# Kernel optimization log

Hardware: AMD Instinct MI355X
Metric: run time of the kernel (lower is better)

## Reference

```python
import jax, jax.numpy as jnp
import numpy as np

B, S, D, H = 4, 2048, 1024, 16
HD = D // H
EPS = 1e-5

def layernorm(x, g, b):
    mu = jnp.mean(x, axis=-1, keepdims=True)
    var = jnp.mean((x - mu) ** 2, axis=-1, keepdims=True)
    return (x - mu) * jax.lax.rsqrt(var + EPS) * g + b

def setup_inputs() -> dict:
    key = jax.random.key(0)
    ks = jax.random.split(key, 12)
    s = 0.02
    return {
        "x": jax.random.normal(ks[0], (B, S, D), dtype=jnp.float32),
        "g1": jnp.ones((D,), jnp.float32), "beta1": jnp.zeros((D,), jnp.float32),
        "Wq": jax.random.normal(ks[1], (H, HD, HD), jnp.float32) * s,
        "bq": jnp.zeros((H, HD), jnp.float32),
        "Wk": jax.random.normal(ks[2], (H, HD, HD), jnp.float32) * s,
        "bk": jnp.zeros((H, HD), jnp.float32),
        "Wv": jax.random.normal(ks[3], (H, HD, HD), jnp.float32) * s,
        "bv": jnp.zeros((H, HD), jnp.float32),
        "Wp": jax.random.normal(ks[4], (D, D), jnp.float32) * s,
        "bp": jnp.zeros((D,), jnp.float32),
        "g2": jnp.ones((D,), jnp.float32), "beta2": jnp.zeros((D,), jnp.float32),
        "W1": jax.random.normal(ks[5], (4 * D, D), jnp.float32) * s,
        "b1": jnp.zeros((4 * D,), jnp.float32),
        "W2": jax.random.normal(ks[6], (D, 4 * D), jnp.float32) * s,
        "b2": jnp.zeros((D,), jnp.float32),
    }

def reference(x, g1, beta1, Wq, bq, Wk, bk, Wv, bv, Wp, bp, g2, beta2, W1, b1, W2, b2):
    # pre-norm
    h = layernorm(x, g1, beta1)              # [B,S,D]
    hh = h.reshape(B, S, H, HD)              # per-head slices of d_model
    # per-head linear: y = x @ W.T + b (torch Linear convention)
    q = jnp.einsum('bshd,hed->bshe', hh, Wq) + bq
    k = jnp.einsum('bshd,hed->bshe', hh, Wk) + bk
    v = jnp.einsum('bshd,hed->bshe', hh, Wv) + bv
    scores = jnp.einsum('bshe,bthe->bhst', q, k) / jnp.sqrt(jnp.float32(HD))
    causal = jnp.tril(jnp.ones((S, S), bool))
    scores = jnp.where(causal, scores, -jnp.inf)
    w = jax.nn.softmax(scores, axis=-1)      # [B,H,S,S]
    attn = jnp.einsum('bhst,bthd->bshd', w, v).reshape(B, S, D)
    out = attn @ Wp.T + bp
    x = x + out
    h2 = layernorm(x, g2, beta2)
    ff = jax.nn.gelu(h2 @ W1.T + b1, approximate=False) @ W2.T + b2
    return x + ff
```

## Files before the change

### kernel.cpp

```cpp
#include <hip/hip_runtime.h>

#define TOK 8192
#define DMODEL 1024
#define NHEAD 16
#define SEQ 2048
#define HDIM 64
#define NQB 16

typedef __attribute__((ext_vector_type(8))) short short8;
typedef __attribute__((ext_vector_type(4))) float f32x4;

__device__ __forceinline__ ushort f2bf(float f){
  unsigned int u = __float_as_uint(f);
  u = u + 0x7fffu + ((u >> 16) & 1u);
  return (ushort)(u >> 16);
}

__device__ __forceinline__ void gld16(const void* g, void* l){
  __builtin_amdgcn_global_load_lds((const __attribute__((address_space(1))) unsigned int*)g,
                                   (__attribute__((address_space(3))) unsigned int*)l, 16, 0, 0);
}

__global__ __launch_bounds__(256) void cvt_kernel(const float* __restrict__ src, ushort* __restrict__ dst, int n4){
  int i = blockIdx.x * 256 + threadIdx.x;
  if(i < n4){
    float4 v = ((const float4*)src)[i];
    ushort4 o;
    o.x = f2bf(v.x); o.y = f2bf(v.y); o.z = f2bf(v.z); o.w = f2bf(v.w);
    ((ushort4*)dst)[i] = o;
  }
}

__device__ __forceinline__ float waveRedSum(float v){
  #pragma unroll
  for(int off = 32; off; off >>= 1) v += __shfl_xor(v, off);
  return v;
}

__global__ __launch_bounds__(256) void ln_kernel(const float* __restrict__ x, const float* __restrict__ g,
                                                 const float* __restrict__ bt, ushort* __restrict__ out){
  int row = blockIdx.x, t = threadIdx.x;
  float4 v = ((const float4*)(x + (size_t)row * DMODEL))[t];
  float s  = v.x + v.y + v.z + v.w;
  float sq = v.x*v.x + v.y*v.y + v.z*v.z + v.w*v.w;
  s = waveRedSum(s); sq = waveRedSum(sq);
  __shared__ float ss[4], ssq[4];
  if((t & 63) == 0){ ss[t >> 6] = s; ssq[t >> 6] = sq; }
  __syncthreads();
  float S  = ss[0] + ss[1] + ss[2] + ss[3];
  float SQ = ssq[0] + ssq[1] + ssq[2] + ssq[3];
  float mean = S * (1.f / DMODEL);
  float var  = SQ * (1.f / DMODEL) - mean * mean;
  float rstd = rsqrtf(var + 1e-5f);
  float4 gv = ((const float4*)g)[t];
  float4 bv = ((const float4*)bt)[t];
  ushort4 o;
  o.x = f2bf((v.x - mean) * rstd * gv.x + bv.x);
  o.y = f2bf((v.y - mean) * rstd * gv.y + bv.y);
  o.z = f2bf((v.z - mean) * rstd * gv.z + bv.z);
  o.w = f2bf((v.w - mean) * rstd * gv.w + bv.w);
  ((ushort4*)(out + (size_t)row * DMODEL))[t] = o;
}

__global__ __launch_bounds__(256) void qkv_kernel(const ushort* __restrict__ h, const ushort* __restrict__ wqkv,
                                                  const float* __restrict__ bq, const float* __restrict__ bk,
                                                  const float* __restrict__ bv,
                                                  ushort* __restrict__ q, ushort* __restrict__ k, ushort* __restrict__ vT){
  __shared__ __attribute__((aligned(16))) ushort hs[64 * 72];
  __shared__ __attribute__((aligned(16))) ushort wsh[3][64 * 72];
  int head = blockIdx.y;
  int tb = blockIdx.x * 64;
  int t = threadIdx.x;
  int r = t >> 2, c0 = (t & 3) * 16;
  {
    const uint4* src = (const uint4*)(h + (size_t)(tb + r) * DMODEL + head * 64 + c0);
    uint4 p0 = src[0], p1 = src[1];
    *(uint4*)&hs[r * 72 + c0] = p0;
    *(uint4*)&hs[r * 72 + c0 + 8] = p1;
  }
  #pragma unroll
  for(int o = 0; o < 3; o++){
    const uint4* wsrc = (const uint4*)(wqkv + ((size_t)(o * NHEAD + head) * 64 + r) * 64 + c0);
    uint4 a0 = wsrc[0], a1 = wsrc[1];
    *(uint4*)&wsh[o][r * 72 + c0] = a0;
    *(uint4*)&wsh[o][r * 72 + c0 + 8] = a1;
  }
  __syncthreads();
  int w = t >> 6, l = t & 63, lr = l & 15, lg = l >> 4;
  short8 a0 = *(const short8*)&hs[(w * 16 + lr) * 72 + lg * 8];
  short8 a1 = *(const short8*)&hs[(w * 16 + lr) * 72 + 32 + lg * 8];
  const float* biases[3] = {bq, bk, bv};
  ushort* outs[2] = {q, k};
  #pragma unroll
  for(int o = 0; o < 3; o++){
    #pragma unroll
    for(int nt = 0; nt < 4; nt++){
      f32x4 acc = {0.f, 0.f, 0.f, 0.f};
      short8 b0 = *(const short8*)&wsh[o][(nt * 16 + lr) * 72 + lg * 8];
      short8 b1 = *(const short8*)&wsh[o][(nt * 16 + lr) * 72 + 32 + lg * 8];
      acc = __builtin_amdgcn_mfma_f32_16x16x32_bf16(a0, b0, acc, 0, 0, 0);
      acc = __builtin_amdgcn_mfma_f32_16x16x32_bf16(a1, b1, acc, 0, 0, 0);
      float bias = biases[o][head * 64 + nt * 16 + lr];
      #pragma unroll
      for(int rr = 0; rr < 4; rr++){
        int tok = tb + w * 16 + lg * 4 + rr;
        int b_ = tok >> 11, s_ = tok & (SEQ - 1);
        if(o < 2){
          outs[o][((size_t)(b_ * NHEAD + head) * SEQ + s_) * 64 + nt * 16 + lr] = f2bf(acc[rr] + bias);
        } else {
          vT[((size_t)(b_ * NHEAD + head) * 64 + nt * 16 + lr) * SEQ + s_] = f2bf(acc[rr] + bias);
        }
      }
    }
  }
}

__global__ __launch_bounds__(256) void attn_kernel(const ushort* __restrict__ q, const ushort* __restrict__ k,
                                                   const ushort* __restrict__ vT, ushort* __restrict__ attn){
  __shared__ __attribute__((aligned(16))) ushort kt[2][64 * 64];
  __shared__ __attribute__((aligned(16))) ushort vt[2][64 * 64];
  __shared__ __attribute__((aligned(16))) ushort pt[4 * 32 * 72];
  int lid = blockIdx.y * 16 + blockIdx.x;
  int qb = (NQB - 1) - (lid >> 6);
  int bh = lid & 63;
  int t = threadIdx.x, w = t >> 6, l = t & 63, lr = l & 15, lg = l >> 4;
  size_t base = (size_t)bh * SEQ * 64;
  int b_ = bh >> 4, head = bh & 15;

  int r8 = l >> 3, c8 = l & 7;
  int st_row = 8 * w + r8;
  int st_sc  = ((c8 ^ r8) << 3);
  int st_dst = w * 1024 + l * 16;
  int xm  = (lr & 7) << 3;
  int cb0 = (lg * 8) ^ xm;
  int cb1 = (32 + lg * 8) ^ xm;

  const float C = 0.18033688f;

  int cur = 0;
  int qbase = qb * 128;
  int wrow = qbase + w * 32;

  short8 qf[2][2];
  #pragma unroll
  for(int mt = 0; mt < 2; mt++)
    #pragma unroll
    for(int kc = 0; kc < 2; kc++)
      qf[mt][kc] = *(const short8*)&q[base + (size_t)(wrow + mt * 16 + lr) * 64 + kc * 32 + lg * 8];

  f32x4 acc_o[2][4];
  #pragma unroll
  for(int i = 0; i < 2; i++)
    #pragma unroll
    for(int jj = 0; jj < 4; jj++) acc_o[i][jj] = (f32x4){0.f, 0.f, 0.f, 0.f};
  float m_sw[2] = {-__builtin_inff(), -__builtin_inff()};
  float l_sw[2] = {0.f, 0.f};

  int jmax = (qbase + 128) >> 6;
  {
    const ushort* kp = k + base + (size_t)st_row * 64 + st_sc;
    char* kd = (char*)&kt[cur][0] + st_dst;
    gld16(kp, kd);
    gld16(kp + 32 * 64, kd + 4096);
    const ushort* vp = vT + base + (size_t)st_row * SEQ + st_sc;
    char* vd = (char*)&vt[cur][0] + st_dst;
    gld16(vp, vd);
    gld16(vp + 32 * SEQ, vd + 4096);
  }
  #pragma unroll 1
  for(int j = 0; j < jmax; j++){
    __syncthreads();
    if(j + 1 < jmax){
      int kb2 = (j + 1) * 64;
      const ushort* kp = k + base + (size_t)(kb2 + st_row) * 64 + st_sc;
      char* kd = (char*)&kt[cur ^ 1][0] + st_dst;
      gld16(kp, kd);
      gld16(kp + 32 * 64, kd + 4096);
      const ushort* vp = vT + base + (size_t)st_row * SEQ + kb2 + st_sc;
      char* vd = (char*)&vt[cur ^ 1][0] + st_dst;
      gld16(vp, vd);
      gld16(vp + 32 * SEQ, vd + 4096);
    }
    int kb = j * 64;
    if(kb <= wrow + 31){
      f32x4 sacc[2][4];
      #pragma unroll
      for(int nt = 0; nt < 4; nt++){
        short8 b0 = *(const short8*)&kt[cur][(nt * 16 + lr) * 64 + cb0];
        short8 b1 = *(const short8*)&kt[cur][(nt * 16 + lr) * 64 + cb1];
        #pragma unroll
        for(int mt = 0; mt < 2; mt++){
          f32x4 z = (f32x4){0.f, 0.f, 0.f, 0.f};
          z = __builtin_amdgcn_mfma_f32_16x16x32_bf16(b0, qf[mt][0], z, 0, 0, 0);
          z = __builtin_amdgcn_mfma_f32_16x16x32_bf16(b1, qf[mt][1], z, 0, 0, 0);
          sacc[mt][nt] = z;
        }
      }
      if(kb + 63 > wrow){
        #pragma unroll
        for(int mt = 0; mt < 2; mt++)
          #pragma unroll
          for(int nt = 0; nt < 4; nt++)
            #pragma unroll
            for(int rr = 0; rr < 4; rr++){
              int kcol = kb + nt * 16 + lg * 4 + rr;
              int qrow = wrow + mt * 16 + lr;
              if(kcol > qrow) sacc[mt][nt][rr] = -__builtin_inff();
            }
      }
      #pragma unroll
      for(int mt = 0; mt < 2; mt++){
        float tm = sacc[mt][0][0];
        #pragma unroll
        for(int nt = 0; nt < 4; nt++)
          #pragma unroll
          for(int rr = 0; rr < 4; rr++) tm = fmaxf(tm, sacc[mt][nt][rr]);
        tm = fmaxf(tm, __shfl_xor(tm, 16));
        tm = fmaxf(tm, __shfl_xor(tm, 32));
        float nm = fmaxf(m_sw[mt], tm);
        if(__any((nm - m_sw[mt]) > 44.0f)){
          float sc = exp2f((m_sw[mt] - nm) * C);
          l_sw[mt] *= sc;
          m_sw[mt] = nm;
          #pragma unroll
          for(int rr = 0; rr < 4; rr++){
            float scb = __shfl(sc, lg * 4 + rr, 16);
            #pragma unroll
            for(int nt = 0; nt < 4; nt++) acc_o[mt][nt][rr] *= scb;
          }
        }
        float mC = m_sw[mt] * C;
        float rs = 0.f;
        #pragma unroll
        for(int nt = 0; nt < 4; nt++){
          float p0 = exp2f(fmaf(sacc[mt][nt][0], C, -mC));
          float p1 = exp2f(fmaf(sacc[mt][nt][1], C, -mC));
          float p2 = exp2f(fmaf(sacc[mt][nt][2], C, -mC));
          float p3 = exp2f(fmaf(sacc[mt][nt][3], C, -mC));
          rs += (p0 + p1) + (p2 + p3);
          ushort4 pw;
          pw.x = f2bf(p0); pw.y = f2bf(p1); pw.z = f2bf(p2); pw.w = f2bf(p3);
          *(ushort4*)&pt[w * 2304 + (mt * 16 + lr) * 72 + nt * 16 + lg * 4] = pw;
        }
        rs += __shfl_xor(rs, 16);
        rs += __shfl_xor(rs, 32);
        l_sw[mt] += rs;
      }
      #pragma unroll
      for(int kc = 0; kc < 2; kc++){
        short8 pf[2];
        #pragma unroll
        for(int mt = 0; mt < 2; mt++)
          pf[mt] = *(const short8*)&pt[w * 2304 + (mt * 16 + lr) * 72 + kc * 32 + lg * 8];
        int cb = kc ? cb1 : cb0;
        #pragma unroll
        for(int nt = 0; nt < 4; nt++){
          short8 vb = *(const short8*)&vt[cur][(nt * 16 + lr) * 64 + cb];
          #pragma unroll
          for(int mt = 0; mt < 2; mt++)
            acc_o[mt][nt] = __builtin_amdgcn_mfma_f32_16x16x32_bf16(pf[mt], vb, acc_o[mt][nt], 0, 0, 0);
        }
      }
    }
    cur ^= 1;
  }
  #pragma unroll
  for(int mt = 0; mt < 2; mt++){
    float inv = 1.f / l_sw[mt];
    #pragma unroll
    for(int rr = 0; rr < 4; rr++){
      float invb = __shfl(inv, lg * 4 + rr, 16);
      #pragma unroll
      for(int nt = 0; nt < 4; nt++){
        int s_ = wrow + mt * 16 + lg * 4 + rr;
        attn[((size_t)(b_ * SEQ + s_)) * DMODEL + head * 64 + nt * 16 + lr] = f2bf(acc_o[mt][nt][rr] * invb);
      }
    }
  }
}

__device__ __forceinline__ float gelu_exact(float x){
  return 0.5f * x * (1.f + erff(x * 0.70710678118654752f));
}

template<int EPI>
__global__ __launch_bounds__(512, 2) void gemm3(const ushort* __restrict__ A, const ushort* __restrict__ W,
                                                const float* __restrict__ bias, const float* __restrict__ res,
                                                float* __restrict__ outf, ushort* __restrict__ outb,
                                                int M, int N, int K){
  __shared__ __attribute__((aligned(16))) ushort As[3][256 * 64];
  __shared__ __attribute__((aligned(16))) ushort Bs[3][128 * 64];
  int t = threadIdx.x;
  int nwg = gridDim.x * gridDim.y;
  int id = blockIdx.y * gridDim.x + blockIdx.x;
  int bx = blockIdx.x, by = blockIdx.y;
  if((nwg & 7) == 0){
    int qq = nwg >> 3;
    int sw = (id & 7) * qq + (id >> 3);
    bx = sw % gridDim.x; by = sw / gridDim.x;
  }
  int n0 = bx * 128, m0 = by * 256;
  int w = t >> 6, l = t & 63, lr = l & 15, lg = l >> 4;
  int wm = w >> 1, wn = w & 1;
  int ur = t >> 3, u = t & 7;
  int su = (u ^ (ur & 7)) << 3;

  f32x4 acc[4][4];
  #pragma unroll
  for(int i = 0; i < 4; i++)
    #pragma unroll
    for(int j = 0; j < 4; j++) acc[i][j] = (f32x4){0.f, 0.f, 0.f, 0.f};

  int ktiles = K >> 6;

  auto stage = [&](int tile){
    int b = tile % 3;
    int k0 = tile << 6;
    char* ad = (char*)&As[b][0] + t * 16;
    char* bd = (char*)&Bs[b][0] + t * 16;
    #pragma unroll
    for(int i = 0; i < 4; i++){
      int ra = i * 64 + ur;
      gld16(A + (size_t)(m0 + ra) * K + k0 + su, ad + i * 8192);
    }
    #pragma unroll
    for(int i = 0; i < 2; i++){
      int rb = i * 64 + ur;
      gld16(W + (size_t)(n0 + rb) * K + k0 + su, bd + i * 8192);
    }
  };

  stage(0);
  stage(1);

  int xm = (lr & 7) << 3;
  int arow = wm * 64, brow = wn * 64;

  #pragma unroll 1
  for(int kt = 0; kt < ktiles; kt++){
    int b = kt % 3;
    if(kt + 2 < ktiles) stage(kt + 2);
    int rem = ktiles - 1 - kt;
    __builtin_amdgcn_sched_barrier(0);
    if(rem >= 2)      asm volatile("s_waitcnt vmcnt(12)" ::: "memory");
    else if(rem == 1) asm volatile("s_waitcnt vmcnt(6)" ::: "memory");
    else              asm volatile("s_waitcnt vmcnt(0)" ::: "memory");
    __builtin_amdgcn_sched_barrier(0);
    __builtin_amdgcn_s_barrier();

    short8 af[4][2], bf[4][2];
    #pragma unroll
    for(int mf = 0; mf < 4; mf++)
      #pragma unroll
      for(int kk = 0; kk < 2; kk++)
        af[mf][kk] = *(const short8*)&As[b][(arow + mf * 16 + lr) * 64 + ((kk * 32 + lg * 8) ^ xm)];
    #pragma unroll
    for(int nf = 0; nf < 4; nf++)
      #pragma unroll
      for(int kk = 0; kk < 2; kk++)
        bf[nf][kk] = *(const short8*)&Bs[b][(brow + nf * 16 + lr) * 64 + ((kk * 32 + lg * 8) ^ xm)];

    __builtin_amdgcn_s_setprio(1);
    #pragma unroll
    for(int mf = 0; mf < 4; mf++)
      #pragma unroll
      for(int nf = 0; nf < 4; nf++){
        acc[mf][nf] = __builtin_amdgcn_mfma_f32_16x16x32_bf16(af[mf][0], bf[nf][0], acc[mf][nf], 0, 0, 0);
        acc[mf][nf] = __builtin_amdgcn_mfma_f32_16x16x32_bf16(af[mf][1], bf[nf][1], acc[mf][nf], 0, 0, 0);
      }
    __builtin_amdgcn_s_setprio(0);

    asm volatile("s_waitcnt lgkmcnt(0)" ::: "memory");
    __builtin_amdgcn_sched_barrier(0);
    __builtin_amdgcn_s_barrier();
  }

  #pragma unroll
  for(int mf = 0; mf < 4; mf++)
    #pragma unroll
    for(int nf = 0; nf < 4; nf++){
      int col = n0 + wn * 64 + nf * 16 + lr;
      float bv = bias[col];
      #pragma unroll
      for(int rr = 0; rr < 4; rr++){
        int row = m0 + wm * 64 + mf * 16 + lg * 4 + rr;
        float val = acc[mf][nf][rr] + bv;
        if(EPI == 0){
          outf[(size_t)row * N + col] = val + res[(size_t)row * N + col];
        } else {
          outb[(size_t)row * N + col] = f2bf(gelu_exact(val));
        }
      }
    }
}

extern "C" void kernel_launch(void* const* d_in, const int* in_sizes, int n_in,
                              void* d_out, int out_size, void* d_ws, size_t ws_size,
                              hipStream_t stream){
  const float* x   = (const float*)d_in[0];
  const float* g1  = (const float*)d_in[1];
  const float* be1 = (const float*)d_in[2];
  const float* Wq  = (const float*)d_in[3];
  const float* bq  = (const float*)d_in[4];
  const float* Wk  = (const float*)d_in[5];
  const float* bk  = (const float*)d_in[6];
  const float* Wv  = (const float*)d_in[7];
  const float* bv  = (const float*)d_in[8];
  const float* Wp  = (const float*)d_in[9];
  const float* bp  = (const float*)d_in[10];
  const float* g2  = (const float*)d_in[11];
  const float* be2 = (const float*)d_in[12];
  const float* W1  = (const float*)d_in[13];
  const float* b1  = (const float*)d_in[14];
  const float* W2  = (const float*)d_in[15];
  const float* b2  = (const float*)d_in[16];
  float* out = (float*)d_out;
  char* ws = (char*)d_ws;

  ushort* wqkv = (ushort*)(ws + 0);
  ushort* wp   = (ushort*)(ws + 393216);
  ushort* w1   = (ushort*)(ws + 2490368);
  ushort* w2   = (ushort*)(ws + 10878976);
  ushort* hbuf = (ushort*)(ws + 19267584);
  ushort* qbuf = (ushort*)(ws + 36044800);
  ushort* kbuf = (ushort*)(ws + 52822016);
  ushort* vTbuf= (ushort*)(ws + 69599232);
  ushort* ff1  = (ushort*)(ws + 86376448);
  ushort* attnb = hbuf;
  ushort* h2 = qbuf;

  cvt_kernel<<<64, 256, 0, stream>>>(Wq, wqkv, 16384);
  cvt_kernel<<<64, 256, 0, stream>>>(Wk, wqkv + 65536, 16384);
  cvt_kernel<<<64, 256, 0, stream>>>(Wv, wqkv + 131072, 16384);
  cvt_kernel<<<1024, 256, 0, stream>>>(Wp, wp, 262144);
  cvt_kernel<<<4096, 256, 0, stream>>>(W1, w1, 1048576);
  cvt_kernel<<<4096, 256, 0, stream>>>(W2, w2, 1048576);

  ln_kernel<<<TOK, 256, 0, stream>>>(x, g1, be1, hbuf);
  qkv_kernel<<<dim3(TOK / 64, NHEAD), 256, 0, stream>>>(hbuf, wqkv, bq, bk, bv, qbuf, kbuf, vTbuf);
  attn_kernel<<<dim3(16, 64), 256, 0, stream>>>(qbuf, kbuf, vTbuf, attnb);
  gemm3<0><<<dim3(8, 32), 512, 0, stream>>>(attnb, wp, bp, x, out, nullptr, 8192, 1024, 1024);
  ln_kernel<<<TOK, 256, 0, stream>>>(out, g2, be2, h2);
  if(ws_size >= 153485312ull){
    gemm3<1><<<dim3(32, 32), 512, 0, stream>>>(h2, w1, b1, nullptr, nullptr, ff1, 8192, 4096, 1024);
    gemm3<0><<<dim3(8, 32), 512, 0, stream>>>(ff1, w2, b2, out, out, nullptr, 8192, 1024, 4096);
  } else {
    for(int c = 0; c < 4; c++){
      gemm3<1><<<dim3(32, 8), 512, 0, stream>>>(h2 + (size_t)c * 2048 * 1024, w1, b1, nullptr, nullptr, ff1,
                                                2048, 4096, 1024);
      gemm3<0><<<dim3(8, 8), 512, 0, stream>>>(ff1, w2, b2, out + (size_t)c * 2048 * 1024,
                                               out + (size_t)c * 2048 * 1024, nullptr, 2048, 1024, 4096);
    }
  }
}
```

Measured before the change: 389.3 us.

## Double-buffer GEMM fragments in registers and deepen global prefetch to three tiles

Rewrites the gemm main loop to prefetch three k-tiles up front and alternate two register fragment sets. LDS reads for the next tile are issued before the MFMAs of the current tile, and one barrier per tile is removed. This aims to hide LDS latency and global load latency behind matrix core work. It raises register pressure and drops the two-blocks-per-CU launch bound hint, which may reduce occupancy.

```diff
diff --git a/kernel.cpp b/kernel.cpp
--- a/kernel.cpp
+++ b/kernel.cpp
@@ -284,10 +284,10 @@
 }
 
 template<int EPI>
-__global__ __launch_bounds__(512, 2) void gemm3(const ushort* __restrict__ A, const ushort* __restrict__ W,
-                                                const float* __restrict__ bias, const float* __restrict__ res,
-                                                float* __restrict__ outf, ushort* __restrict__ outb,
-                                                int M, int N, int K){
+__global__ __launch_bounds__(512) void gemmrp(const ushort* __restrict__ A, const ushort* __restrict__ W,
+                                              const float* __restrict__ bias, const float* __restrict__ res,
+                                              float* __restrict__ outf, ushort* __restrict__ outb,
+                                              int M, int N, int K){
   __shared__ __attribute__((aligned(16))) ushort As[3][256 * 64];
   __shared__ __attribute__((aligned(16))) ushort Bs[3][128 * 64];
   int t = threadIdx.x;
@@ -330,49 +330,62 @@
     }
   };
 
-  stage(0);
-  stage(1);
-
   int xm = (lr & 7) << 3;
   int arow = wm * 64, brow = wn * 64;
 
+  short8 fa0[4][2], fb0[4][2], fa1[4][2], fb1[4][2];
+
+  auto rdf = [&](int b, short8 (&fa)[4][2], short8 (&fb)[4][2]){
+    #pragma unroll
+    for(int mf = 0; mf < 4; mf++)
+      #pragma unroll
+      for(int kk = 0; kk < 2; kk++)
+        fa[mf][kk] = *(const short8*)&As[b][(arow + mf * 16 + lr) * 64 + ((kk * 32 + lg * 8) ^ xm)];
+    #pragma unroll
+    for(int nf = 0; nf < 4; nf++)
+      #pragma unroll
+      for(int kk = 0; kk < 2; kk++)
+        fb[nf][kk] = *(const short8*)&Bs[b][(brow + nf * 16 + lr) * 64 + ((kk * 32 + lg * 8) ^ xm)];
+  };
+  auto mmac = [&](short8 (&fa)[4][2], short8 (&fb)[4][2]){
+    __builtin_amdgcn_s_setprio(1);
+    #pragma unroll
+    for(int mf = 0; mf < 4; mf++)
+      #pragma unroll
+      for(int nf = 0; nf < 4; nf++){
+        acc[mf][nf] = __builtin_amdgcn_mfma_f32_16x16x32_bf16(fa[mf][0], fb[nf][0], acc[mf][nf], 0, 0, 0);
+        acc[mf][nf] = __builtin_amdgcn_mfma_f32_16x16x32_bf16(fa[mf][1], fb[nf][1], acc[mf][nf], 0, 0, 0);
+      }
+    __builtin_amdgcn_s_setprio(0);
+  };
+
+  stage(0); stage(1); stage(2);
+  asm volatile("s_waitcnt vmcnt(12)" ::: "memory");
+  __builtin_amdgcn_sched_barrier(0);
+  __builtin_amdgcn_s_barrier();
+  __builtin_amdgcn_sched_barrier(0);
+  rdf(0, fa0, fb0);
+
   #pragma unroll 1
-  for(int kt = 0; kt < ktiles; kt++){
-    int b = kt % 3;
-    if(kt + 2 < ktiles) stage(kt + 2);
-    int rem = ktiles - 1 - kt;
-    __builtin_amdgcn_sched_barrier(0);
-    if(rem >= 2)      asm volatile("s_waitcnt vmcnt(12)" ::: "memory");
-    else if(rem == 1) asm volatile("s_waitcnt vmcnt(6)" ::: "memory");
-    else              asm volatile("s_waitcnt vmcnt(0)" ::: "memory");
+  for(int kt = 0; kt < ktiles; kt += 2){
+    if(kt + 2 < ktiles) asm volatile("s_waitcnt vmcnt(6) lgkmcnt(0)" ::: "memory");
+    else                asm volatile("s_waitcnt vmcnt(0) lgkmcnt(0)" ::: "memory");
     __builtin_amdgcn_sched_barrier(0);
     __builtin_amdgcn_s_barrier();
-
-    short8 af[4][2], bf[4][2];
-    #pragma unroll
-    for(int mf = 0; mf < 4; mf++)
-      #pragma unroll
-      for(int kk = 0; kk < 2; kk++)
-        af[mf][kk] = *(const short8*)&As[b][(arow + mf * 16 + lr) * 64 + ((kk * 32 + lg * 8) ^ xm)];
-    #pragma unroll
-    for(int nf = 0; nf < 4; nf++)
-      #pragma unroll
-      for(int kk = 0; kk < 2; kk++)
-        bf[nf][kk] = *(const short8*)&Bs[b][(brow + nf * 16 + lr) * 64 + ((kk * 32 + lg * 8) ^ xm)];
-
-    __builtin_amdgcn_s_setprio(1);
-    #pragma unroll
-    for(int mf = 0; mf < 4; mf++)
-      #pragma unroll
-      for(int nf = 0; nf < 4; nf++){
-        acc[mf][nf] = __builtin_amdgcn_mfma_f32_16x16x32_bf16(af[mf][0], bf[nf][0], acc[mf][nf], 0, 0, 0);
-        acc[mf][nf] = __builtin_amdgcn_mfma_f32_16x16x32_bf16(af[mf][1], bf[nf][1], acc[mf][nf], 0, 0, 0);
-      }
-    __builtin_amdgcn_s_setprio(0);
-
-    asm volatile("s_waitcnt lgkmcnt(0)" ::: "memory");
     __builtin_amdgcn_sched_barrier(0);
-    __builtin_amdgcn_s_barrier();
+    if(kt + 3 < ktiles) stage(kt + 3);
+    if(kt + 1 < ktiles) rdf((kt + 1) % 3, fa1, fb1);
+    mmac(fa0, fb0);
+    if(kt + 1 < ktiles){
+      if(kt + 3 < ktiles) asm volatile("s_waitcnt vmcnt(6) lgkmcnt(0)" ::: "memory");
+      else                asm volatile("s_waitcnt vmcnt(0) lgkmcnt(0)" ::: "memory");
+      __builtin_amdgcn_sched_barrier(0);
+      __builtin_amdgcn_s_barrier();
+      __builtin_amdgcn_sched_barrier(0);
+      if(kt + 4 < ktiles) stage(kt + 4);
+      if(kt + 2 < ktiles) rdf((kt + 2) % 3, fa0, fb0);
+      mmac(fa1, fb1);
+    }
   }
 
   #pragma unroll
@@ -439,17 +452,17 @@
   ln_kernel<<<TOK, 256, 0, stream>>>(x, g1, be1, hbuf);
   qkv_kernel<<<dim3(TOK / 64, NHEAD), 256, 0, stream>>>(hbuf, wqkv, bq, bk, bv, qbuf, kbuf, vTbuf);
   attn_kernel<<<dim3(16, 64), 256, 0, stream>>>(qbuf, kbuf, vTbuf, attnb);
-  gemm3<0><<<dim3(8, 32), 512, 0, stream>>>(attnb, wp, bp, x, out, nullptr, 8192, 1024, 1024);
+  gemmrp<0><<<dim3(8, 32), 512, 0, stream>>>(attnb, wp, bp, x, out, nullptr, 8192, 1024, 1024);
   ln_kernel<<<TOK, 256, 0, stream>>>(out, g2, be2, h2);
   if(ws_size >= 153485312ull){
-    gemm3<1><<<dim3(32, 32), 512, 0, stream>>>(h2, w1, b1, nullptr, nullptr, ff1, 8192, 4096, 1024);
-    gemm3<0><<<dim3(8, 32), 512, 0, stream>>>(ff1, w2, b2, out, out, nullptr, 8192, 1024, 4096);
+    gemmrp<1><<<dim3(32, 32), 512, 0, stream>>>(h2, w1, b1, nullptr, nullptr, ff1, 8192, 4096, 1024);
+    gemmrp<0><<<dim3(8, 32), 512, 0, stream>>>(ff1, w2, b2, out, out, nullptr, 8192, 1024, 4096);
   } else {
     for(int c = 0; c < 4; c++){
-      gemm3<1><<<dim3(32, 8), 512, 0, stream>>>(h2 + (size_t)c * 2048 * 1024, w1, b1, nullptr, nullptr, ff1,
-                                                2048, 4096, 1024);
-      gemm3<0><<<dim3(8, 8), 512, 0, stream>>>(ff1, w2, b2, out + (size_t)c * 2048 * 1024,
-                                               out + (size_t)c * 2048 * 1024, nullptr, 2048, 1024, 4096);
-    }
-  }
-}
+      gemmrp<1><<<dim3(32, 8), 512, 0, stream>>>(h2 + (size_t)c * 2048 * 1024, w1, b1, nullptr, nullptr, ff1,
+                                                 2048, 4096, 1024);
+      gemmrp<0><<<dim3(8, 8), 512, 0, stream>>>(ff1, w2, b2, out + (size_t)c * 2048 * 1024,
+                                                out + (size_t)c * 2048 * 1024, nullptr, 2048, 1024, 4096);
+    }
+  }
+}
```

Measured after the change: 388.8 us. Within noise of the previous version (-0.1%).

## Replace 256x128 GEMM with smaller 128x128x32 tile kernel for more occupancy

Applied to the files above, without the earlier changes.

Swaps the 512-thread 256x128 block GEMM with a 64-wide K step for a 256-thread 128x128 block kernel with a 32-wide K step, a new LDS swizzle and three blocks per CU. Each tile uses less LDS, so more workgroups can be resident and the grid has more blocks, which should help latency hiding and load balance across CUs. The cost is more K iterations with a barrier each, fewer MFMAs per barrier, and lower operand reuse per block.

```diff
diff --git a/kernel.cpp b/kernel.cpp
--- a/kernel.cpp
+++ b/kernel.cpp
@@ -284,12 +284,12 @@
 }
 
 template<int EPI>
-__global__ __launch_bounds__(512, 2) void gemm3(const ushort* __restrict__ A, const ushort* __restrict__ W,
-                                                const float* __restrict__ bias, const float* __restrict__ res,
-                                                float* __restrict__ outf, ushort* __restrict__ outb,
-                                                int M, int N, int K){
-  __shared__ __attribute__((aligned(16))) ushort As[3][256 * 64];
-  __shared__ __attribute__((aligned(16))) ushort Bs[3][128 * 64];
+__global__ __launch_bounds__(256, 3) void gemmsm(const ushort* __restrict__ A, const ushort* __restrict__ W,
+                                                 const float* __restrict__ bias, const float* __restrict__ res,
+                                                 float* __restrict__ outf, ushort* __restrict__ outb,
+                                                 int M, int N, int K){
+  __shared__ __attribute__((aligned(16))) ushort As[3][128 * 32];
+  __shared__ __attribute__((aligned(16))) ushort Bs[3][128 * 32];
   int t = threadIdx.x;
   int nwg = gridDim.x * gridDim.y;
   int id = blockIdx.y * gridDim.x + blockIdx.x;
@@ -299,11 +299,9 @@
     int sw = (id & 7) * qq + (id >> 3);
     bx = sw % gridDim.x; by = sw / gridDim.x;
   }
-  int n0 = bx * 128, m0 = by * 256;
+  int n0 = bx * 128, m0 = by * 128;
   int w = t >> 6, l = t & 63, lr = l & 15, lg = l >> 4;
   int wm = w >> 1, wn = w & 1;
-  int ur = t >> 3, u = t & 7;
-  int su = (u ^ (ur & 7)) << 3;
 
   f32x4 acc[4][4];
   #pragma unroll
@@ -311,29 +309,26 @@
     #pragma unroll
     for(int j = 0; j < 4; j++) acc[i][j] = (f32x4){0.f, 0.f, 0.f, 0.f};
 
-  int ktiles = K >> 6;
+  int ktiles = K >> 5;
+  int srow = t >> 2;
+  int ssc = (((t & 3) ^ ((srow >> 1) & 3)) << 3);
 
   auto stage = [&](int tile){
     int b = tile % 3;
-    int k0 = tile << 6;
+    int k0 = tile << 5;
+    const ushort* Ap = A + (size_t)(m0 + srow) * K + k0 + ssc;
+    const ushort* Bp = W + (size_t)(n0 + srow) * K + k0 + ssc;
     char* ad = (char*)&As[b][0] + t * 16;
     char* bd = (char*)&Bs[b][0] + t * 16;
-    #pragma unroll
-    for(int i = 0; i < 4; i++){
-      int ra = i * 64 + ur;
-      gld16(A + (size_t)(m0 + ra) * K + k0 + su, ad + i * 8192);
-    }
-    #pragma unroll
-    for(int i = 0; i < 2; i++){
-      int rb = i * 64 + ur;
-      gld16(W + (size_t)(n0 + rb) * K + k0 + su, bd + i * 8192);
-    }
+    gld16(Ap, ad);
+    gld16(Ap + (size_t)64 * K, ad + 4096);
+    gld16(Bp, bd);
+    gld16(Bp + (size_t)64 * K, bd + 4096);
   };
 
   stage(0);
   stage(1);
 
-  int xm = (lr & 7) << 3;
   int arow = wm * 64, brow = wn * 64;
 
   #pragma unroll 1
@@ -342,32 +337,30 @@
     if(kt + 2 < ktiles) stage(kt + 2);
     int rem = ktiles - 1 - kt;
     __builtin_amdgcn_sched_barrier(0);
-    if(rem >= 2)      asm volatile("s_waitcnt vmcnt(12)" ::: "memory");
-    else if(rem == 1) asm volatile("s_waitcnt vmcnt(6)" ::: "memory");
+    if(rem >= 2)      asm volatile("s_waitcnt vmcnt(8)" ::: "memory");
+    else if(rem == 1) asm volatile("s_waitcnt vmcnt(4)" ::: "memory");
     else              asm volatile("s_waitcnt vmcnt(0)" ::: "memory");
     __builtin_amdgcn_sched_barrier(0);
     __builtin_amdgcn_s_barrier();
 
-    short8 af[4][2], bf[4][2];
+    short8 af[4], bf[4];
+    #pragma unroll
+    for(int mf = 0; mf < 4; mf++){
+      int R = arow + mf * 16 + lr;
+      af[mf] = *(const short8*)&As[b][R * 32 + ((lg ^ ((R >> 1) & 3)) << 3)];
+    }
+    #pragma unroll
+    for(int nf = 0; nf < 4; nf++){
+      int R = brow + nf * 16 + lr;
+      bf[nf] = *(const short8*)&Bs[b][R * 32 + ((lg ^ ((R >> 1) & 3)) << 3)];
+    }
+
+    __builtin_amdgcn_s_setprio(1);
     #pragma unroll
     for(int mf = 0; mf < 4; mf++)
       #pragma unroll
-      for(int kk = 0; kk < 2; kk++)
-        af[mf][kk] = *(const short8*)&As[b][(arow + mf * 16 + lr) * 64 + ((kk * 32 + lg * 8) ^ xm)];
-    #pragma unroll
-    for(int nf = 0; nf < 4; nf++)
-      #pragma unroll
-      for(int kk = 0; kk < 2; kk++)
-        bf[nf][kk] = *(const short8*)&Bs[b][(brow + nf * 16 + lr) * 64 + ((kk * 32 + lg * 8) ^ xm)];
-
-    __builtin_amdgcn_s_setprio(1);
-    #pragma unroll
-    for(int mf = 0; mf < 4; mf++)
-      #pragma unroll
-      for(int nf = 0; nf < 4; nf++){
-        acc[mf][nf] = __builtin_amdgcn_mfma_f32_16x16x32_bf16(af[mf][0], bf[nf][0], acc[mf][nf], 0, 0, 0);
-        acc[mf][nf] = __builtin_amdgcn_mfma_f32_16x16x32_bf16(af[mf][1], bf[nf][1], acc[mf][nf], 0, 0, 0);
-      }
+      for(int nf = 0; nf < 4; nf++)
+        acc[mf][nf] = __builtin_amdgcn_mfma_f32_16x16x32_bf16(af[mf], bf[nf], acc[mf][nf], 0, 0, 0);
     __builtin_amdgcn_s_setprio(0);
 
     asm volatile("s_waitcnt lgkmcnt(0)" ::: "memory");
@@ -439,17 +432,17 @@
   ln_kernel<<<TOK, 256, 0, stream>>>(x, g1, be1, hbuf);
   qkv_kernel<<<dim3(TOK / 64, NHEAD), 256, 0, stream>>>(hbuf, wqkv, bq, bk, bv, qbuf, kbuf, vTbuf);
   attn_kernel<<<dim3(16, 64), 256, 0, stream>>>(qbuf, kbuf, vTbuf, attnb);
-  gemm3<0><<<dim3(8, 32), 512, 0, stream>>>(attnb, wp, bp, x, out, nullptr, 8192, 1024, 1024);
+  gemmsm<0><<<dim3(8, 64), 256, 0, stream>>>(attnb, wp, bp, x, out, nullptr, 8192, 1024, 1024);
   ln_kernel<<<TOK, 256, 0, stream>>>(out, g2, be2, h2);
   if(ws_size >= 153485312ull){
-    gemm3<1><<<dim3(32, 32), 512, 0, stream>>>(h2, w1, b1, nullptr, nullptr, ff1, 8192, 4096, 1024);
-    gemm3<0><<<dim3(8, 32), 512, 0, stream>>>(ff1, w2, b2, out, out, nullptr, 8192, 1024, 4096);
+    gemmsm<1><<<dim3(32, 64), 256, 0, stream>>>(h2, w1, b1, nullptr, nullptr, ff1, 8192, 4096, 1024);
+    gemmsm<0><<<dim3(8, 64), 256, 0, stream>>>(ff1, w2, b2, out, out, nullptr, 8192, 1024, 4096);
   } else {
     for(int c = 0; c < 4; c++){
-      gemm3<1><<<dim3(32, 8), 512, 0, stream>>>(h2 + (size_t)c * 2048 * 1024, w1, b1, nullptr, nullptr, ff1,
-                                                2048, 4096, 1024);
-      gemm3<0><<<dim3(8, 8), 512, 0, stream>>>(ff1, w2, b2, out + (size_t)c * 2048 * 1024,
-                                               out + (size_t)c * 2048 * 1024, nullptr, 2048, 1024, 4096);
-    }
-  }
-}
+      gemmsm<1><<<dim3(32, 16), 256, 0, stream>>>(h2 + (size_t)c * 2048 * 1024, w1, b1, nullptr, nullptr, ff1,
+                                                  2048, 4096, 1024);
+      gemmsm<0><<<dim3(8, 16), 256, 0, stream>>>(ff1, w2, b2, out + (size_t)c * 2048 * 1024,
+                                                 out + (size_t)c * 2048 * 1024, nullptr, 2048, 1024, 4096);
+    }
+  }
+}
```

Result: faster. 373.5 us (-4.1%).
